# Performance work log

Hardware: AMD Instinct MI355X
Metric: run time of the kernel (lower is better)

Reference implementation:

```python
import jax, jax.numpy as jnp
import numpy as np
from jax import lax

V, D, P, C = 151936, 1024, 64, 28
B, S = 1, 1024
EPS = 1.1920929e-07  # torch.finfo(float32).eps, used by nn.RMSNorm(eps=None)


def setup_inputs() -> dict:
    key = jax.random.key(0)
    ks = jax.random.split(key, 10)
    return {
        "tokens": jax.random.randint(ks[0], (B, S), 0, V),
        "embed_table": jax.random.normal(ks[1], (V, D), jnp.float32) * 0.02,
        "plane_proj_w": jax.random.normal(ks[2], (C, 2 * P, D), jnp.float32) * (1.0 / np.sqrt(D)),
        "back_proj_w": jax.random.normal(ks[3], (C, D, 2 * P), jnp.float32) * 0.02,
        "base_angles": jax.random.normal(ks[4], (C, P), jnp.float32) * 0.1,
        "angle_gen_w": jax.random.normal(ks[5], (P, D), jnp.float32) * 0.01,
        "scales": jnp.ones((C, D), jnp.float32),
        "shifts": jnp.zeros((C, D), jnp.float32),
        "norm_w": jnp.ones((C, D), jnp.float32),
        "decay_param": jnp.float32(0.9),
        "gate_w": jax.random.normal(ks[6], (D, D), jnp.float32) * 0.02,
        "out_norm_w": jnp.ones((D,), jnp.float32),
        "lm_head_w": jax.random.normal(ks[7], (V, D), jnp.float32) * 0.02,
    }


def _rms_norm(v, w):
    return v * lax.rsqrt(jnp.mean(v * v, axis=-1, keepdims=True) + EPS) * w


def _causal_mix(x, decay_param, gate_w):
    # state_t = d*state_{t-1} + (1-d)*x_t, causal EMA over sequence
    d = jax.nn.sigmoid(decay_param)
    def step(s, xt):
        s = d * s + (1.0 - d) * xt
        return s, s
    _, ys = lax.scan(step, jnp.zeros(x.shape[::2], x.dtype)[0:0].sum(0) + jnp.zeros((x.shape[0], x.shape[2]), x.dtype), jnp.swapaxes(x, 0, 1))
    causal = jnp.swapaxes(ys, 0, 1)  # [B,S,D]
    return x + causal @ gate_w.T


def reference(tokens, embed_table, plane_proj_w, back_proj_w, base_angles,
              angle_gen_w, scales, shifts, norm_w, decay_param, gate_w,
              out_norm_w, lm_head_w):
    x = embed_table[tokens].astype(jnp.float32)  # [B,S,D]
    n_cycles = scales.shape[0]
    for i in range(n_cycles):
        # input-dependent angle offset (detached in the original)
        extra = x.mean(axis=1) @ angle_gen_w.T          # [B,P]
        angles = base_angles[i] + lax.stop_gradient(extra.mean(axis=0)) * 0.1
        if i % 4 == 0:
            x = _causal_mix(x, decay_param, gate_w)
        # learned-plane rotation
        proj = x @ plane_proj_w[i].T                     # [B,S,2P]
        n = proj.shape[-1] // 2
        a, b = proj[..., :n], proj[..., n:]
        ca, sa = jnp.cos(angles), jnp.sin(angles)
        rot = jnp.concatenate([a * ca - b * sa, a * sa + b * ca], axis=-1)
        x_rot = x + rot @ back_proj_w[i].T
        x_act = jax.nn.silu(x_rot * scales[i] + shifts[i])
        x = x + _rms_norm(x_act - x, norm_w[i])
    x = _rms_norm(x, out_norm_w)
    return x @ lm_head_w.T  # [B,S,V]
```

## Files before the change

### kernel.cpp

```cpp
#include <hip/hip_runtime.h>

typedef __attribute__((ext_vector_type(4))) float f32x4;
typedef __attribute__((ext_vector_type(8))) short bf16x8;
typedef unsigned short u16;
typedef unsigned int u32;
typedef __attribute__((ext_vector_type(4))) unsigned short u16x4;

#define EPS 1.1920929e-07f
#define S 1024
#define D 1024
#define NV 151936
#define NCYC 28
#define SMEM_BYTES 49152

__device__ __forceinline__ u16 f2bf(float f) {
  u32 u = __float_as_uint(f);
  return (u16)((u + 0x7fffu + ((u >> 16) & 1u)) >> 16);
}
__device__ __forceinline__ float bf2f(u16 h) {
  return __uint_as_float((u32)h << 16);
}
struct bfpair { u16 h, l; };
__device__ __forceinline__ bfpair split_bf(float v) {
  bfpair r;
  r.h = f2bf(v);
  r.l = f2bf(v - bf2f(r.h));
  return r;
}

__device__ __forceinline__ void gl16(const void* g, void* s) {
  __builtin_amdgcn_global_load_lds((const __attribute__((address_space(1))) u32*)g,
                                   (__attribute__((address_space(3))) u32*)s, 16, 0, 0);
}

__device__ __forceinline__ float block_sum256(float v, float* sbuf) {
  #pragma unroll
  for (int off = 32; off; off >>= 1) v += __shfl_down(v, off);
  int lane = threadIdx.x & 63, w = threadIdx.x >> 6;
  __syncthreads();
  if (lane == 0) sbuf[w] = v;
  __syncthreads();
  return sbuf[0] + sbuf[1] + sbuf[2] + sbuf[3];
}

__global__ void k_cvt(const float* __restrict__ src, u16* __restrict__ dst, size_t n4) {
  size_t i = (size_t)blockIdx.x * 256 + threadIdx.x;
  size_t stride = (size_t)gridDim.x * 256;
  for (; i < n4; i += stride) {
    f32x4 v = ((const f32x4*)src)[i];
    u16x4 o;
    #pragma unroll
    for (int e = 0; e < 4; ++e) o[e] = f2bf(v[e]);
    ((u16x4*)dst)[i] = o;
  }
}

__global__ void k_cvt2(const float* __restrict__ src, u16* __restrict__ dh,
                       u16* __restrict__ dl, size_t n4) {
  size_t i = (size_t)blockIdx.x * 256 + threadIdx.x;
  size_t stride = (size_t)gridDim.x * 256;
  for (; i < n4; i += stride) {
    f32x4 v = ((const f32x4*)src)[i];
    u16x4 oh, ol;
    #pragma unroll
    for (int e = 0; e < 4; ++e) { bfpair p = split_bf(v[e]); oh[e] = p.h; ol[e] = p.l; }
    ((u16x4*)dh)[i] = oh;
    ((u16x4*)dl)[i] = ol;
  }
}

__device__ void side_cvt(const float* __restrict__ src, u16* __restrict__ dst,
                         int chunk, int blkbase) {
  const size_t n4 = (size_t)NV * D / 4;
  const size_t per = (n4 + (size_t)(NCYC * 3) - 1) / (size_t)(NCYC * 3);
  size_t lo = (size_t)chunk * per;
  size_t hi = lo + per;
  if (hi > n4) hi = n4;
  const size_t nb = (size_t)(gridDim.x - blkbase);
  for (size_t i = lo + (size_t)(blockIdx.x - blkbase) * 256 + threadIdx.x; i < hi;
       i += nb * 256) {
    f32x4 v = ((const f32x4*)src)[i];
    u16x4 o;
    #pragma unroll
    for (int e = 0; e < 4; ++e) o[e] = f2bf(v[e]);
    ((u16x4*)dst)[i] = o;
  }
}


__device__ void gather_phase(const int* tokens, const float* embed,
                             float* x, u16* xh, u16* xl, float* cp) {
  const int t = threadIdx.x;
  if (blockIdx.x >= 256) return;
  f32x4 creg = 0.f;
  for (int rr = 0; rr < 4; ++rr) {
    int s = blockIdx.x * 4 + rr;
    int tok = tokens[s];
    f32x4 v = ((const f32x4*)(embed + (size_t)tok * D))[t];
    u16x4 oh, ol;
    #pragma unroll
    for (int e = 0; e < 4; ++e) { bfpair p = split_bf(v[e]); oh[e] = p.h; ol[e] = p.l; }
    ((f32x4*)(x + (size_t)s * D))[t] = v;
    ((u16x4*)(xh + (size_t)s * D))[t] = oh;
    ((u16x4*)(xl + (size_t)s * D))[t] = ol;
    creg += v;
  }
  *(f32x4*)(cp + (size_t)blockIdx.x * D + t * 4) = creg;
}

template <bool CADD>
__device__ void gemm64_phase(char* smem, const u16* Ah_, const u16* Al_,
                             const u16* Bh_, const u16* Bl_, int K,
                             float* xout, u16* xho, u16* xlo, float* Cout, int G) {
  const int t = threadIdx.x;
  u16* Ash = (u16*)smem;
  u16* Asl = Ash + 4096;
  u16* Bsh = Asl + 4096;
  u16* Bsl = Bsh + 4096;
  const int wave = t >> 6, lane = t & 63;
  const int fr = lane & 15, kb = lane >> 4;
  const int sr = t >> 3, skc = (t & 7) << 3;
  const int sswz = skc ^ ((sr & 7) << 3);
  for (int tile = blockIdx.x; tile < 256; tile += G) {
    const int m0 = (tile >> 4) * 64, n0 = (tile & 15) * 64;
    f32x4 acc[4];
    #pragma unroll
    for (int j = 0; j < 4; ++j) acc[j] = 0.f;

    for (int k0 = 0; k0 < K; k0 += 64) {
      #pragma unroll
      for (int it = 0; it < 2; ++it) {
        int r = it * 32 + sr;
        size_t ga = (size_t)(m0 + r) * K + k0 + sswz;
        size_t gb = (size_t)(n0 + r) * K + k0 + sswz;
        int so = r * 64 + skc;
        gl16(Ah_ + ga, Ash + so);
        gl16(Al_ + ga, Asl + so);
        gl16(Bh_ + gb, Bsh + so);
        gl16(Bl_ + gb, Bsl + so);
      }
      __syncthreads();
      #pragma unroll
      for (int ks = 0; ks < 2; ++ks) {
        const int cphys = (ks * 32 + kb * 8) ^ ((fr & 7) << 3);
        int oa = (wave * 16 + fr) * 64 + cphys;
        bf16x8 ah = *(const bf16x8*)&Ash[oa];
        bf16x8 al = *(const bf16x8*)&Asl[oa];
        #pragma unroll
        for (int j = 0; j < 4; ++j) {
          int ob = (j * 16 + fr) * 64 + cphys;
          bf16x8 bh = *(const bf16x8*)&Bsh[ob];
          bf16x8 bl = *(const bf16x8*)&Bsl[ob];
          acc[j] = __builtin_amdgcn_mfma_f32_16x16x32_bf16(ah, bh, acc[j], 0, 0, 0);
          acc[j] = __builtin_amdgcn_mfma_f32_16x16x32_bf16(ah, bl, acc[j], 0, 0, 0);
          acc[j] = __builtin_amdgcn_mfma_f32_16x16x32_bf16(al, bh, acc[j], 0, 0, 0);
        }
      }
      __syncthreads();
    }
    #pragma unroll
    for (int j = 0; j < 4; ++j)
      #pragma unroll
      for (int rg = 0; rg < 4; ++rg) {
        int m = m0 + wave * 16 + kb * 4 + rg;
        int n = n0 + j * 16 + fr;
        if (CADD) {
          float v = xout[(size_t)m * D + n] + acc[j][rg];
          xout[(size_t)m * D + n] = v;
          bfpair p = split_bf(v);
          xho[(size_t)m * D + n] = p.h;
          xlo[(size_t)m * D + n] = p.l;
        } else {
          Cout[(size_t)m * D + n] = acc[j][rg];
        }
      }
  }
}

__device__ void causal_phase(char* smem, const float* x, u16* Rh, u16* Rl,
                             float dec, int G) {
  const int t = threadIdx.x;
  for (int tile = blockIdx.x; tile < 256; tile += G) {
    int s0 = (tile >> 4) * 64, d0 = (tile & 15) * 64;
    float (*tl)[64] = (float(*)[64])smem;
    for (int idx = t; idx < 159 * 64; idx += 256) {
      int rr = idx >> 6, c = idx & 63;
      int gs = s0 - 95 + rr;
      tl[rr][c] = (gs >= 0) ? x[(size_t)gs * D + d0 + c] : 0.f;
    }
    __syncthreads();
    int c = t & 63, r0 = t >> 6;
    for (int rr = r0; rr < 64; rr += 4) {
      float acc = 0.f, w = 1.f - dec;
      int base = rr + 95;
      #pragma unroll 8
      for (int j = 0; j < 96; ++j) { acc += w * tl[base - j][c]; w *= dec; }
      bfpair p = split_bf(acc);
      Rh[(size_t)(s0 + rr) * D + d0 + c] = p.h;
      Rl[(size_t)(s0 + rr) * D + d0 + c] = p.l;
    }
    __syncthreads();
  }
}

__device__ void proj_phase(char* smem, const u16* xh, const u16* xl,
                           const u16* Bh_, const u16* Bl_, float* pacc) {
  const int t = threadIdx.x;
  const int mt = blockIdx.x & 15, kq = blockIdx.x >> 4;
  const int m0 = mt * 64;
  const int k0 = kq * 64;
  u16* Ash = (u16*)smem;
  u16* Asl = Ash + 4096;
  u16* Bsh = Asl + 4096;
  u16* Bsl = Bsh + 8192;
  const int wave = t >> 6, lane = t & 63;
  const int fr = lane & 15, kb = lane >> 4;
  const int sr = t >> 3, skc = (t & 7) << 3;
  const int sswz = skc ^ ((sr & 7) << 3);
  f32x4 acc[8];
  #pragma unroll
  for (int j = 0; j < 8; ++j) acc[j] = 0.f;

  #pragma unroll
  for (int it = 0; it < 2; ++it) {
    int r = it * 32 + sr;
    size_t ga = (size_t)(m0 + r) * D + k0 + sswz;
    gl16(xh + ga, Ash + r * 64 + skc);
    gl16(xl + ga, Asl + r * 64 + skc);
  }
  #pragma unroll
  for (int it = 0; it < 4; ++it) {
    int r = it * 32 + sr;
    size_t gb = (size_t)r * D + k0 + sswz;
    gl16(Bh_ + gb, Bsh + r * 64 + skc);
    gl16(Bl_ + gb, Bsl + r * 64 + skc);
  }
  __syncthreads();
  #pragma unroll
  for (int ks = 0; ks < 2; ++ks) {
    const int cphys = (ks * 32 + kb * 8) ^ ((fr & 7) << 3);
    int oa = (wave * 16 + fr) * 64 + cphys;
    bf16x8 ah = *(const bf16x8*)&Ash[oa];
    bf16x8 al = *(const bf16x8*)&Asl[oa];
    #pragma unroll
    for (int j = 0; j < 8; ++j) {
      int ob = (j * 16 + fr) * 64 + cphys;
      bf16x8 bh = *(const bf16x8*)&Bsh[ob];
      bf16x8 bl = *(const bf16x8*)&Bsl[ob];
      acc[j] = __builtin_amdgcn_mfma_f32_16x16x32_bf16(ah, bh, acc[j], 0, 0, 0);
      acc[j] = __builtin_amdgcn_mfma_f32_16x16x32_bf16(ah, bl, acc[j], 0, 0, 0);
      acc[j] = __builtin_amdgcn_mfma_f32_16x16x32_bf16(al, bh, acc[j], 0, 0, 0);
    }
  }
  float* pb = pacc + (size_t)blockIdx.x * 64 * 128;
  #pragma unroll
  for (int j = 0; j < 8; ++j)
    #pragma unroll
    for (int rg = 0; rg < 4; ++rg) {
      int ml = wave * 16 + kb * 4 + rg;
      pb[ml * 128 + j * 16 + fr] = acc[j][rg];
    }
}

__device__ void angles_all(float* colsum, const float* cp, const float* agw,
                           const float* bang_i, float* trig) {
  const int t = threadIdx.x;
  f32x4 acc = 0.f;
  for (int b = 0; b < 256; ++b)
    acc += *(const f32x4*)(cp + (size_t)b * D + t * 4);
  *(f32x4*)&colsum[t * 4] = acc;
  __syncthreads();
  const int wave = t >> 6, lane = t & 63;
  for (int pp = 0; pp < 16; ++pp) {
    int p = wave * 16 + pp;
    float sum = 0.f;
    #pragma unroll
    for (int q = 0; q < 16; ++q) {
      int d = lane + q * 64;
      sum += colsum[d] * agw[p * D + d];
    }
    #pragma unroll
    for (int off = 32; off; off >>= 1) sum += __shfl_down(sum, off);
    if (lane == 0) {
      float ang = bang_i[p] + 0.1f * (sum * (1.f / (float)S));
      trig[p] = cosf(ang);
      trig[64 + p] = sinf(ang);
    }
  }
}

__device__ void epilogue_phase(float* sbuf, float* x, u16* xh, u16* xl,
                               const float* Rf, const float* scale,
                               const float* shift, const float* nw, float* cp) {
  const int t = threadIdx.x;
  f32x4 sc = *(const f32x4*)(scale + t * 4);
  f32x4 sh = *(const f32x4*)(shift + t * 4);
  f32x4 nwv = *(const f32x4*)(nw + t * 4);
  f32x4 creg = 0.f;
  for (int rr = 0; rr < 4; ++rr) {
    int s = blockIdx.x * 4 + rr;
    f32x4 xv = *(const f32x4*)(x + (size_t)s * D + t * 4);
    f32x4 rv = *(const f32x4*)(Rf + (size_t)s * D + t * 4);
    float y[4], ss = 0.f;
    #pragma unroll
    for (int c = 0; c < 4; ++c) {
      float xr = xv[c] + rv[c];
      float tt = xr * sc[c] + sh[c];
      float act = tt / (1.f + expf(-tt));
      y[c] = act - xv[c];
      ss += y[c] * y[c];
    }
    float total = block_sum256(ss, sbuf);
    float inv = rsqrtf(total * (1.f / (float)D) + EPS);
    f32x4 o;
    u16x4 oh, ol;
    #pragma unroll
    for (int c = 0; c < 4; ++c) {
      o[c] = xv[c] + y[c] * inv * nwv[c];
      bfpair p = split_bf(o[c]);
      oh[c] = p.h;
      ol[c] = p.l;
      creg[c] += o[c];
    }
    *(f32x4*)(x + (size_t)s * D + t * 4) = o;
    *(u16x4*)(xh + (size_t)s * D + t * 4) = oh;
    *(u16x4*)(xl + (size_t)s * D + t * 4) = ol;
  }
  *(f32x4*)(cp + (size_t)blockIdx.x * D + t * 4) = creg;
}

__device__ void outnorm_phase(float* sbuf, const float* x, const float* w, u16* xn) {
  const int t = threadIdx.x;
  if (blockIdx.x >= 256) return;
  for (int rr = 0; rr < 4; ++rr) {
    int s = blockIdx.x * 4 + rr;
    f32x4 xv = *(const f32x4*)(x + (size_t)s * D + t * 4);
    float total = block_sum256(xv[0]*xv[0] + xv[1]*xv[1] + xv[2]*xv[2] + xv[3]*xv[3], sbuf);
    float inv = rsqrtf(total * (1.f / (float)D) + EPS);
    f32x4 wv = *(const f32x4*)(w + t * 4);
    u16x4 o;
    #pragma unroll
    for (int c = 0; c < 4; ++c) o[c] = f2bf(xv[c] * inv * wv[c]);
    *(u16x4*)(xn + (size_t)s * D + t * 4) = o;
  }
}

__global__ __launch_bounds__(256) void fb_gather(const int* tokens, const float* embed,
                                                 float* x, u16* xh, u16* xl, float* cp) {
  gather_phase(tokens, embed, x, xh, xl, cp);
}
__global__ __launch_bounds__(256) void fb_causal(const float* x, u16* Rh, u16* Rl,
                                                 const float* decay) {
  __shared__ __align__(16) char sm[40704];
  causal_phase(sm, x, Rh, Rl, 1.f / (1.f + expf(-decay[0])), gridDim.x);
}
__global__ __launch_bounds__(256) void fb_gate(const u16* Rh, const u16* Rl,
                                               const u16* gh, const u16* gl,
                                               float* x, u16* xh, u16* xl) {
  __shared__ __align__(16) char sm[32768];
  gemm64_phase<true>(sm, Rh, Rl, gh, gl, 1024, x, xh, xl, nullptr, gridDim.x);
}
__global__ __launch_bounds__(256) void fb_proj(const u16* xh, const u16* xl,
                                               const u16* Wph, const u16* Wpl,
                                               const float* cp, const float* agw,
                                               const float* bang_i,
                                               float* pacc, float* trig,
                                               const float* lmw, u16* lm_bf, int chunk) {
  __shared__ __align__(16) char sm[SMEM_BYTES];
  if (blockIdx.x < 256) proj_phase(sm, xh, xl, Wph, Wpl, pacc);
  else if (blockIdx.x == 256) angles_all((float*)sm, cp, agw, bang_i, trig);
  else side_cvt(lmw, lm_bf, chunk, 257);
}

__global__ __launch_bounds__(256) void fb_back(const float* __restrict__ pacc,
                                               const float* __restrict__ trig,
                                               const u16* __restrict__ Bh_,
                                               const u16* __restrict__ Bl_,
                                               float* __restrict__ Rf,
                                               const float* lmw, u16* lm_bf, int chunk) {
  __shared__ u16 Ash[64 * 128];
  __shared__ u16 Asl[64 * 128];
  __shared__ u16 Bsh[64 * 64];
  __shared__ u16 Bsl[64 * 64];
  if (blockIdx.x >= 256) { side_cvt(lmw, lm_bf, chunk, 256); return; }
  const int t = threadIdx.x;
  const int tile = blockIdx.x;
  const int mt = tile >> 4;
  const int m0 = mt * 64, n0 = (tile & 15) * 64;
  const int wave = t >> 6, lane = t & 63;
  const int fr = lane & 15, kb = lane >> 4;
  const int sr = t >> 3, skc = (t & 7) << 3;
  const int sswz = skc ^ ((sr & 7) << 3);

  #pragma unroll
  for (int ri = 0; ri < 2; ++ri) {
    int r = ri * 32 + sr;
    int pdst = skc ^ ((r & 7) << 3);
    f32x4 a0 = 0.f, a1 = 0.f, b0 = 0.f, b1 = 0.f;
    #pragma unroll
    for (int kq = 0; kq < 16; ++kq) {
      const float* pk = pacc + ((size_t)(kq * 16 + mt) * 64 + r) * 128;
      a0 += *(const f32x4*)(pk + skc);
      a1 += *(const f32x4*)(pk + skc + 4);
      b0 += *(const f32x4*)(pk + 64 + skc);
      b1 += *(const f32x4*)(pk + 64 + skc + 4);
    }
    #pragma unroll
    for (int kh = 0; kh < 2; ++kh) {
      u16 hbuf[8], lbuf[8];
      #pragma unroll
      for (int j = 0; j < 8; ++j) {
        float av = (j < 4) ? a0[j & 3] : a1[j & 3];
        float bv = (j < 4) ? b0[j & 3] : b1[j & 3];
        float ca = trig[skc + j], sa = trig[64 + skc + j];
        float v = (kh == 0) ? (av * ca - bv * sa) : (av * sa + bv * ca);
        bfpair p = split_bf(v);
        hbuf[j] = p.h;
        lbuf[j] = p.l;
      }
      int so = r * 128 + kh * 64 + pdst;
      *(bf16x8*)&Ash[so] = *(bf16x8*)hbuf;
      *(bf16x8*)&Asl[so] = *(bf16x8*)lbuf;
    }
  }
  __syncthreads();

  f32x4 acc[4];
  #pragma unroll
  for (int j = 0; j < 4; ++j) acc[j] = 0.f;

  for (int kt = 0; kt < 2; ++kt) {
    int k0 = kt * 64;
    #pragma unroll
    for (int it = 0; it < 2; ++it) {
      int r = it * 32 + sr;
      size_t gb = (size_t)(n0 + r) * 128 + k0 + sswz;
      gl16(Bh_ + gb, Bsh + r * 64 + skc);
      gl16(Bl_ + gb, Bsl + r * 64 + skc);
    }
    __syncthreads();
    #pragma unroll
    for (int ks = 0; ks < 2; ++ks) {
      const int w = (ks * 32 + kb * 8) ^ ((fr & 7) << 3);
      int oa = (wave * 16 + fr) * 128 + k0 + w;
      bf16x8 ah = *(const bf16x8*)&Ash[oa];
      bf16x8 al = *(const bf16x8*)&Asl[oa];
      #pragma unroll
      for (int j = 0; j < 4; ++j) {
        int ob = (j * 16 + fr) * 64 + w;
        bf16x8 bh = *(const bf16x8*)&Bsh[ob];
        bf16x8 bl = *(const bf16x8*)&Bsl[ob];
        acc[j] = __builtin_amdgcn_mfma_f32_16x16x32_bf16(ah, bh, acc[j], 0, 0, 0);
        acc[j] = __builtin_amdgcn_mfma_f32_16x16x32_bf16(ah, bl, acc[j], 0, 0, 0);
        acc[j] = __builtin_amdgcn_mfma_f32_16x16x32_bf16(al, bh, acc[j], 0, 0, 0);
      }
    }
    __syncthreads();
  }
  #pragma unroll
  for (int j = 0; j < 4; ++j)
    #pragma unroll
    for (int rg = 0; rg < 4; ++rg) {
      int m = m0 + wave * 16 + kb * 4 + rg;
      int n = n0 + j * 16 + fr;
      Rf[(size_t)m * D + n] = acc[j][rg];
    }
}

__global__ __launch_bounds__(256) void fb_epi(float* x, u16* xh, u16* xl, const float* Rf,
                                              const float* scale, const float* shift,
                                              const float* nw, float* cp,
                                              const float* lmw, u16* lm_bf, int chunk) {
  __shared__ float sbuf[4];
  if (blockIdx.x < 256) epilogue_phase(sbuf, x, xh, xl, Rf, scale, shift, nw, cp);
  else side_cvt(lmw, lm_bf, chunk, 256);
}
__global__ __launch_bounds__(256) void fb_outnorm(const float* x, const float* w, u16* xn) {
  __shared__ float sbuf[4];
  outnorm_phase(sbuf, x, w, xn);
}

template <bool PRECONV>
__global__ __launch_bounds__(256) void k_lm(const u16* __restrict__ A,
                                            const void* __restrict__ Wsrc,
                                            float* __restrict__ out) {
  __shared__ u16 As[2][128 * 64];
  __shared__ u16 Bs[2][128 * 64];
  const int bid = blockIdx.x;
  const int lid = (bid & 7) * 1187 + (bid >> 3);
  const int m0 = (lid & 7) * 128;
  const int n0 = (lid >> 3) * 128;
  const int t = threadIdx.x;
  const int wave = t >> 6, lane = t & 63;
  const int wm = (wave >> 1) * 64, wn = (wave & 1) * 64;
  const int fr = lane & 15, kb = lane >> 4;
  const int sr = t >> 3, skc = (t & 7) << 3;
  const int sswz = skc ^ ((sr & 7) << 3);
  const u16* Wb16 = (const u16*)Wsrc;
  const float* Wf = (const float*)Wsrc;
  f32x4 acc[4][4];
  #pragma unroll
  for (int i = 0; i < 4; ++i)
    #pragma unroll
    for (int j = 0; j < 4; ++j) acc[i][j] = 0.f;

  auto stage = [&](int buf, int k0) {
    #pragma unroll
    for (int it = 0; it < 4; ++it) {
      int r = it * 32 + sr;
      gl16(A + (size_t)(m0 + r) * D + k0 + sswz, &As[buf][r * 64 + skc]);
    }
    if (PRECONV) {
      #pragma unroll
      for (int it = 0; it < 4; ++it) {
        int r = it * 32 + sr;
        gl16(Wb16 + (size_t)(n0 + r) * D + k0 + sswz, &Bs[buf][r * 64 + skc]);
      }
    } else {
      #pragma unroll
      for (int it = 0; it < 4; ++it) {
        int r = it * 32 + sr;
        const float* src = Wf + (size_t)(n0 + r) * D + k0 + sswz;
        f32x4 v0 = *(const f32x4*)src;
        f32x4 v1 = *(const f32x4*)(src + 4);
        u16 h[8];
        #pragma unroll
        for (int e = 0; e < 4; ++e) { h[e] = f2bf(v0[e]); h[e + 4] = f2bf(v1[e]); }
        *(bf16x8*)&Bs[buf][r * 64 + skc] = *(bf16x8*)h;
      }
    }
  };

  stage(0, 0);
  __syncthreads();
  for (int kt = 0; kt < 16; ++kt) {
    const int cur = kt & 1;
    if (kt < 15) stage(cur ^ 1, (kt + 1) * 64);
    #pragma unroll
    for (int ks = 0; ks < 2; ++ks) {
      const int cphys = (ks * 32 + kb * 8) ^ ((fr & 7) << 3);
      bf16x8 a[4], b[4];
      #pragma unroll
      for (int i = 0; i < 4; ++i) a[i] = *(const bf16x8*)&As[cur][(wm + i * 16 + fr) * 64 + cphys];
      #pragma unroll
      for (int j = 0; j < 4; ++j) b[j] = *(const bf16x8*)&Bs[cur][(wn + j * 16 + fr) * 64 + cphys];
      #pragma unroll
      for (int i = 0; i < 4; ++i)
        #pragma unroll
        for (int j = 0; j < 4; ++j)
          acc[i][j] = __builtin_amdgcn_mfma_f32_16x16x32_bf16(a[i], b[j], acc[i][j], 0, 0, 0);
    }
    __syncthreads();
  }
  #pragma unroll
  for (int i = 0; i < 4; ++i)
    #pragma unroll
    for (int j = 0; j < 4; ++j)
      #pragma unroll
      for (int rg = 0; rg < 4; ++rg) {
        int m = m0 + wm + i * 16 + kb * 4 + rg;
        int n = n0 + wn + j * 16 + fr;
        out[(size_t)m * NV + n] = acc[i][j][rg];
      }
}

extern "C" void kernel_launch(void* const* d_in, const int* in_sizes, int n_in,
                              void* d_out, int out_size, void* d_ws, size_t ws_size,
                              hipStream_t stream) {
  const int* tokens = (const int*)d_in[0];
  const float* embed = (const float*)d_in[1];
  const float* Wp = (const float*)d_in[2];
  const float* Wb = (const float*)d_in[3];
  const float* bang = (const float*)d_in[4];
  const float* agw = (const float*)d_in[5];
  const float* scales = (const float*)d_in[6];
  const float* shifts = (const float*)d_in[7];
  const float* normw = (const float*)d_in[8];
  const float* decay = (const float*)d_in[9];
  const float* gatew = (const float*)d_in[10];
  const float* onorm = (const float*)d_in[11];
  const float* lmw = (const float*)d_in[12];
  float* out = (float*)d_out;

  char* ws = (char*)d_ws;
  const size_t MB = 1u << 20;
  float* x = (float*)ws;
  u16* xh = (u16*)(ws + 4 * MB);
  u16* xl = (u16*)(ws + 6 * MB);
  float* Rf = (float*)(ws + 8 * MB);
  u16* Rh = (u16*)(ws + 12 * MB);
  u16* Rl = (u16*)(ws + 14 * MB);
  float* trig = (float*)(ws + 16 * MB);
  float* cp = (float*)(ws + 17 * MB);
  u16* xn = (u16*)(ws + 20 * MB);
  u16* gate_h = (u16*)(ws + 22 * MB);
  u16* gate_l = (u16*)(ws + 24 * MB);
  u16* Wp_h = (u16*)(ws + 26 * MB);
  u16* Wp_l = (u16*)(ws + 33 * MB);
  u16* Wb_h = (u16*)(ws + 40 * MB);
  u16* Wb_l = (u16*)(ws + 47 * MB);
  float* pacc = (float*)(ws + 54 * MB);
  u16* lm_bf = (u16*)(ws + 62 * MB);

  const size_t lm_elems = (size_t)NV * D;
  bool preconv = ws_size >= 62 * MB + lm_elems * 2;
  const float* side_src = preconv ? lmw : nullptr;
  u16* side_dst = preconv ? lm_bf : nullptr;
  const int gproj = preconv ? 385 : 257;
  const int gside = preconv ? 384 : 256;

  k_cvt2<<<512, 256, 0, stream>>>(gatew, gate_h, gate_l, (size_t)D * D / 4);
  k_cvt2<<<1024, 256, 0, stream>>>(Wp, Wp_h, Wp_l, (size_t)NCYC * 128 * D / 4);
  k_cvt2<<<1024, 256, 0, stream>>>(Wb, Wb_h, Wb_l, (size_t)NCYC * 128 * D / 4);

  fb_gather<<<256, 256, 0, stream>>>(tokens, embed, x, xh, xl, cp);
  for (int i = 0; i < NCYC; ++i) {
    const u16* Wph = Wp_h + (size_t)i * 128 * D;
    const u16* Wpl = Wp_l + (size_t)i * 128 * D;
    const u16* Wbh = Wb_h + (size_t)i * 128 * D;
    const u16* Wbl = Wb_l + (size_t)i * 128 * D;
    if ((i & 3) == 0) {
      fb_causal<<<256, 256, 0, stream>>>(x, Rh, Rl, decay);
      fb_gate<<<256, 256, 0, stream>>>(Rh, Rl, gate_h, gate_l, x, xh, xl);
    }
    fb_proj<<<gproj, 256, 0, stream>>>(xh, xl, Wph, Wpl, cp, agw, bang + i * 64,
                                       pacc, trig, side_src, side_dst, i * 3);
    fb_back<<<gside, 256, 0, stream>>>(pacc, trig, Wbh, Wbl, Rf,
                                       side_src, side_dst, i * 3 + 1);
    fb_epi<<<gside, 256, 0, stream>>>(x, xh, xl, Rf, scales + i * D, shifts + i * D,
                                      normw + i * D, cp, side_src, side_dst, i * 3 + 2);
  }
  fb_outnorm<<<256, 256, 0, stream>>>(x, onorm, xn);

  if (preconv)
    k_lm<true><<<9496, 256, 0, stream>>>(xn, lm_bf, out);
  else
    k_lm<false><<<9496, 256, 0, stream>>>(xn, lmw, out);
}
```

Baseline: 2.925 ms.

## Fuse weight conversions into gather, double-buffer gate GEMM, single-buffer LM head

Folds the three split-bf16 weight conversion launches into the gather kernel by giving extra blocks the conversion ranges, which removes separate launches and lets the conversions overlap the gather. The gate GEMM is rewritten as one tile per block with double-buffered LDS staging (64KB shared), so loads for the next K step overlap MFMA work on the current one. The LM-head kernel goes the other way, from double to single buffering, which halves its LDS footprint (possibly to raise occupancy) but exposes load latency on the largest GEMM.

Result: faster. 2.769 ms (-5.3%).

```diff
diff --git a/kernel.cpp b/kernel.cpp
--- a/kernel.cpp
+++ b/kernel.cpp
@@ -43,23 +43,10 @@
   return sbuf[0] + sbuf[1] + sbuf[2] + sbuf[3];
 }
 
-__global__ void k_cvt(const float* __restrict__ src, u16* __restrict__ dst, size_t n4) {
-  size_t i = (size_t)blockIdx.x * 256 + threadIdx.x;
-  size_t stride = (size_t)gridDim.x * 256;
-  for (; i < n4; i += stride) {
-    f32x4 v = ((const f32x4*)src)[i];
-    u16x4 o;
-    #pragma unroll
-    for (int e = 0; e < 4; ++e) o[e] = f2bf(v[e]);
-    ((u16x4*)dst)[i] = o;
-  }
-}
-
-__global__ void k_cvt2(const float* __restrict__ src, u16* __restrict__ dh,
-                       u16* __restrict__ dl, size_t n4) {
-  size_t i = (size_t)blockIdx.x * 256 + threadIdx.x;
-  size_t stride = (size_t)gridDim.x * 256;
-  for (; i < n4; i += stride) {
+__device__ void cvt2_range(const float* __restrict__ src, u16* __restrict__ dh,
+                           u16* __restrict__ dl, size_t n4, int blkbase, int nblk) {
+  for (size_t i = (size_t)(blockIdx.x - blkbase) * 256 + threadIdx.x; i < n4;
+       i += (size_t)nblk * 256) {
     f32x4 v = ((const f32x4*)src)[i];
     u16x4 oh, ol;
     #pragma unroll
@@ -91,7 +78,6 @@
 __device__ void gather_phase(const int* tokens, const float* embed,
                              float* x, u16* xh, u16* xl, float* cp) {
   const int t = threadIdx.x;
-  if (blockIdx.x >= 256) return;
   f32x4 creg = 0.f;
   for (int rr = 0; rr < 4; ++rr) {
     int s = blockIdx.x * 4 + rr;
@@ -109,72 +95,77 @@
 }
 
 template <bool CADD>
-__device__ void gemm64_phase(char* smem, const u16* Ah_, const u16* Al_,
-                             const u16* Bh_, const u16* Bl_, int K,
-                             float* xout, u16* xho, u16* xlo, float* Cout, int G) {
+__device__ void gemm64_dbuf(char* smem, const u16* Ah_, const u16* Al_,
+                            const u16* Bh_, const u16* Bl_, int K,
+                            float* xout, u16* xho, u16* xlo, float* Cout) {
   const int t = threadIdx.x;
   u16* Ash = (u16*)smem;
-  u16* Asl = Ash + 4096;
-  u16* Bsh = Asl + 4096;
-  u16* Bsl = Bsh + 4096;
+  u16* Asl = Ash + 8192;
+  u16* Bsh = Asl + 8192;
+  u16* Bsl = Bsh + 8192;
   const int wave = t >> 6, lane = t & 63;
   const int fr = lane & 15, kb = lane >> 4;
   const int sr = t >> 3, skc = (t & 7) << 3;
   const int sswz = skc ^ ((sr & 7) << 3);
-  for (int tile = blockIdx.x; tile < 256; tile += G) {
-    const int m0 = (tile >> 4) * 64, n0 = (tile & 15) * 64;
-    f32x4 acc[4];
-    #pragma unroll
-    for (int j = 0; j < 4; ++j) acc[j] = 0.f;
-
-    for (int k0 = 0; k0 < K; k0 += 64) {
-      #pragma unroll
-      for (int it = 0; it < 2; ++it) {
-        int r = it * 32 + sr;
-        size_t ga = (size_t)(m0 + r) * K + k0 + sswz;
-        size_t gb = (size_t)(n0 + r) * K + k0 + sswz;
-        int so = r * 64 + skc;
-        gl16(Ah_ + ga, Ash + so);
-        gl16(Al_ + ga, Asl + so);
-        gl16(Bh_ + gb, Bsh + so);
-        gl16(Bl_ + gb, Bsl + so);
+  const int m0 = (blockIdx.x >> 4) * 64, n0 = (blockIdx.x & 15) * 64;
+  f32x4 acc[4];
+  #pragma unroll
+  for (int j = 0; j < 4; ++j) acc[j] = 0.f;
+
+  auto stage = [&](int buf, int k0) {
+    #pragma unroll
+    for (int it = 0; it < 2; ++it) {
+      int r = it * 32 + sr;
+      size_t ga = (size_t)(m0 + r) * K + k0 + sswz;
+      size_t gb = (size_t)(n0 + r) * K + k0 + sswz;
+      int so = buf * 4096 + r * 64 + skc;
+      gl16(Ah_ + ga, Ash + so);
+      gl16(Al_ + ga, Asl + so);
+      gl16(Bh_ + gb, Bsh + so);
+      gl16(Bl_ + gb, Bsl + so);
+    }
+  };
+  const int nt = K >> 6;
+  stage(0, 0);
+  __syncthreads();
+  for (int kt = 0; kt < nt; ++kt) {
+    const int cur = kt & 1;
+    if (kt + 1 < nt) stage(cur ^ 1, (kt + 1) << 6);
+    const int co = cur * 4096;
+    #pragma unroll
+    for (int ks = 0; ks < 2; ++ks) {
+      const int cphys = (ks * 32 + kb * 8) ^ ((fr & 7) << 3);
+      int oa = co + (wave * 16 + fr) * 64 + cphys;
+      bf16x8 ah = *(const bf16x8*)&Ash[oa];
+      bf16x8 al = *(const bf16x8*)&Asl[oa];
+      #pragma unroll
+      for (int j = 0; j < 4; ++j) {
+        int ob = co + (j * 16 + fr) * 64 + cphys;
+        bf16x8 bh = *(const bf16x8*)&Bsh[ob];
+        bf16x8 bl = *(const bf16x8*)&Bsl[ob];
+        acc[j] = __builtin_amdgcn_mfma_f32_16x16x32_bf16(ah, bh, acc[j], 0, 0, 0);
+        acc[j] = __builtin_amdgcn_mfma_f32_16x16x32_bf16(ah, bl, acc[j], 0, 0, 0);
+        acc[j] = __builtin_amdgcn_mfma_f32_16x16x32_bf16(al, bh, acc[j], 0, 0, 0);
       }
-      __syncthreads();
-      #pragma unroll
-      for (int ks = 0; ks < 2; ++ks) {
-        const int cphys = (ks * 32 + kb * 8) ^ ((fr & 7) << 3);
-        int oa = (wave * 16 + fr) * 64 + cphys;
-        bf16x8 ah = *(const bf16x8*)&Ash[oa];
-        bf16x8 al = *(const bf16x8*)&Asl[oa];
-        #pragma unroll
-        for (int j = 0; j < 4; ++j) {
-          int ob = (j * 16 + fr) * 64 + cphys;
-          bf16x8 bh = *(const bf16x8*)&Bsh[ob];
-          bf16x8 bl = *(const bf16x8*)&Bsl[ob];
-          acc[j] = __builtin_amdgcn_mfma_f32_16x16x32_bf16(ah, bh, acc[j], 0, 0, 0);
-          acc[j] = __builtin_amdgcn_mfma_f32_16x16x32_bf16(ah, bl, acc[j], 0, 0, 0);
-          acc[j] = __builtin_amdgcn_mfma_f32_16x16x32_bf16(al, bh, acc[j], 0, 0, 0);
-        }
+    }
+    __syncthreads();
+  }
+  #pragma unroll
+  for (int j = 0; j < 4; ++j)
+    #pragma unroll
+    for (int rg = 0; rg < 4; ++rg) {
+      int m = m0 + wave * 16 + kb * 4 + rg;
+      int n = n0 + j * 16 + fr;
+      if (CADD) {
+        float v = xout[(size_t)m * D + n] + acc[j][rg];
+        xout[(size_t)m * D + n] = v;
+        bfpair p = split_bf(v);
+        xho[(size_t)m * D + n] = p.h;
+        xlo[(size_t)m * D + n] = p.l;
+      } else {
+        Cout[(size_t)m * D + n] = acc[j][rg];
       }
-      __syncthreads();
-    }
-    #pragma unroll
-    for (int j = 0; j < 4; ++j)
-      #pragma unroll
-      for (int rg = 0; rg < 4; ++rg) {
-        int m = m0 + wave * 16 + kb * 4 + rg;
-        int n = n0 + j * 16 + fr;
-        if (CADD) {
-          float v = xout[(size_t)m * D + n] + acc[j][rg];
-          xout[(size_t)m * D + n] = v;
-          bfpair p = split_bf(v);
-          xho[(size_t)m * D + n] = p.h;
-          xlo[(size_t)m * D + n] = p.l;
-        } else {
-          Cout[(size_t)m * D + n] = acc[j][rg];
-        }
-      }
-  }
+    }
 }
 
 __device__ void causal_phase(char* smem, const float* x, u16* Rh, u16* Rl,
@@ -331,7 +322,6 @@
 
 __device__ void outnorm_phase(float* sbuf, const float* x, const float* w, u16* xn) {
   const int t = threadIdx.x;
-  if (blockIdx.x >= 256) return;
   for (int rr = 0; rr < 4; ++rr) {
     int s = blockIdx.x * 4 + rr;
     f32x4 xv = *(const f32x4*)(x + (size_t)s * D + t * 4);
@@ -346,8 +336,19 @@
 }
 
 __global__ __launch_bounds__(256) void fb_gather(const int* tokens, const float* embed,
-                                                 float* x, u16* xh, u16* xl, float* cp) {
-  gather_phase(tokens, embed, x, xh, xl, cp);
+                                                 float* x, u16* xh, u16* xl, float* cp,
+                                                 const float* gatew, u16* gh, u16* gl,
+                                                 const float* Wp, u16* Wph, u16* Wpl,
+                                                 const float* Wb, u16* Wbh, u16* Wbl) {
+  if (blockIdx.x < 256) {
+    gather_phase(tokens, embed, x, xh, xl, cp);
+  } else if (blockIdx.x < 384) {
+    cvt2_range(gatew, gh, gl, (size_t)D * D / 4, 256, 128);
+  } else if (blockIdx.x < 576) {
+    cvt2_range(Wp, Wph, Wpl, (size_t)NCYC * 128 * D / 4, 384, 192);
+  } else {
+    cvt2_range(Wb, Wbh, Wbl, (size_t)NCYC * 128 * D / 4, 576, 192);
+  }
 }
 __global__ __launch_bounds__(256) void fb_causal(const float* x, u16* Rh, u16* Rl,
                                                  const float* decay) {
@@ -357,8 +358,8 @@
 __global__ __launch_bounds__(256) void fb_gate(const u16* Rh, const u16* Rl,
                                                const u16* gh, const u16* gl,
                                                float* x, u16* xh, u16* xl) {
-  __shared__ __align__(16) char sm[32768];
-  gemm64_phase<true>(sm, Rh, Rl, gh, gl, 1024, x, xh, xl, nullptr, gridDim.x);
+  __shared__ __align__(16) char sm[65536];
+  gemm64_dbuf<true>(sm, Rh, Rl, gh, gl, 1024, x, xh, xl, nullptr);
 }
 __global__ __launch_bounds__(256) void fb_proj(const u16* xh, const u16* xl,
                                                const u16* Wph, const u16* Wpl,
@@ -484,8 +485,8 @@
 __global__ __launch_bounds__(256) void k_lm(const u16* __restrict__ A,
                                             const void* __restrict__ Wsrc,
                                             float* __restrict__ out) {
-  __shared__ u16 As[2][128 * 64];
-  __shared__ u16 Bs[2][128 * 64];
+  __shared__ u16 As[128 * 64];
+  __shared__ u16 Bs[128 * 64];
   const int bid = blockIdx.x;
   const int lid = (bid & 7) * 1187 + (bid >> 3);
   const int m0 = (lid & 7) * 128;
@@ -504,17 +505,17 @@
     #pragma unroll
     for (int j = 0; j < 4; ++j) acc[i][j] = 0.f;
 
-  auto stage = [&](int buf, int k0) {
+  for (int k0 = 0; k0 < D; k0 += 64) {
     #pragma unroll
     for (int it = 0; it < 4; ++it) {
       int r = it * 32 + sr;
-      gl16(A + (size_t)(m0 + r) * D + k0 + sswz, &As[buf][r * 64 + skc]);
+      gl16(A + (size_t)(m0 + r) * D + k0 + sswz, As + r * 64 + skc);
     }
     if (PRECONV) {
       #pragma unroll
       for (int it = 0; it < 4; ++it) {
         int r = it * 32 + sr;
-        gl16(Wb16 + (size_t)(n0 + r) * D + k0 + sswz, &Bs[buf][r * 64 + skc]);
+        gl16(Wb16 + (size_t)(n0 + r) * D + k0 + sswz, Bs + r * 64 + skc);
       }
     } else {
       #pragma unroll
@@ -526,24 +527,18 @@
         u16 h[8];
         #pragma unroll
         for (int e = 0; e < 4; ++e) { h[e] = f2bf(v0[e]); h[e + 4] = f2bf(v1[e]); }
-        *(bf16x8*)&Bs[buf][r * 64 + skc] = *(bf16x8*)h;
+        *(bf16x8*)&Bs[r * 64 + skc] = *(bf16x8*)h;
       }
     }
-  };
-
-  stage(0, 0);
-  __syncthreads();
-  for (int kt = 0; kt < 16; ++kt) {
-    const int cur = kt & 1;
-    if (kt < 15) stage(cur ^ 1, (kt + 1) * 64);
+    __syncthreads();
     #pragma unroll
     for (int ks = 0; ks < 2; ++ks) {
       const int cphys = (ks * 32 + kb * 8) ^ ((fr & 7) << 3);
       bf16x8 a[4], b[4];
       #pragma unroll
-      for (int i = 0; i < 4; ++i) a[i] = *(const bf16x8*)&As[cur][(wm + i * 16 + fr) * 64 + cphys];
-      #pragma unroll
-      for (int j = 0; j < 4; ++j) b[j] = *(const bf16x8*)&Bs[cur][(wn + j * 16 + fr) * 64 + cphys];
+      for (int i = 0; i < 4; ++i) a[i] = *(const bf16x8*)&As[(wm + i * 16 + fr) * 64 + cphys];
+      #pragma unroll
+      for (int j = 0; j < 4; ++j) b[j] = *(const bf16x8*)&Bs[(wn + j * 16 + fr) * 64 + cphys];
       #pragma unroll
       for (int i = 0; i < 4; ++i)
         #pragma unroll
@@ -609,11 +604,9 @@
   const int gproj = preconv ? 385 : 257;
   const int gside = preconv ? 384 : 256;
 
-  k_cvt2<<<512, 256, 0, stream>>>(gatew, gate_h, gate_l, (size_t)D * D / 4);
-  k_cvt2<<<1024, 256, 0, stream>>>(Wp, Wp_h, Wp_l, (size_t)NCYC * 128 * D / 4);
-  k_cvt2<<<1024, 256, 0, stream>>>(Wb, Wb_h, Wb_l, (size_t)NCYC * 128 * D / 4);
-
-  fb_gather<<<256, 256, 0, stream>>>(tokens, embed, x, xh, xl, cp);
+  fb_gather<<<768, 256, 0, stream>>>(tokens, embed, x, xh, xl, cp,
+                                     gatew, gate_h, gate_l,
+                                     Wp, Wp_h, Wp_l, Wb, Wb_h, Wb_l);
   for (int i = 0; i < NCYC; ++i) {
     const u16* Wph = Wp_h + (size_t)i * 128 * D;
     const u16* Wpl = Wp_l + (size_t)i * 128 * D;
```
